# Performance work log

Hardware: AMD Instinct MI355X
Metric: run time of the kernel (lower is better)

## Reference

```python
import jax, jax.numpy as jnp
import numpy as np

NUM_HEADS = 16
THETA = 10000.0


def apply_rope(x, pos, theta):
    # x: [B, H, S, d], pos: [S] int
    d = x.shape[-1]
    inv_freq = theta ** (-jnp.arange(0, d, 2, dtype=jnp.float32) / d)  # [d/2]
    ang = pos.astype(jnp.float32)[:, None] * inv_freq  # [S, d/2]
    cos, sin = jnp.cos(ang), jnp.sin(ang)
    x1, x2 = x[..., 0::2], x[..., 1::2]
    out_even = x1 * cos - x2 * sin
    out_odd = x1 * sin + x2 * cos
    return jnp.stack([out_even, out_odd], axis=-1).reshape(x.shape)


def setup_inputs() -> dict:
    key = jax.random.key(0)
    ks = jax.random.split(key, 5)
    B, S, D = 4, 2048, 2048
    s = 1.0 / np.sqrt(D)
    return {
        "x": jax.random.normal(ks[0], (B, S, D), dtype=jnp.float32),
        "token_positions": jnp.arange(S, dtype=jnp.int32),
        "wq": jax.random.normal(ks[1], (D, D), dtype=jnp.float32) * s,
        "wk": jax.random.normal(ks[2], (D, D), dtype=jnp.float32) * s,
        "wv": jax.random.normal(ks[3], (D, D), dtype=jnp.float32) * s,
        "wo": jax.random.normal(ks[4], (D, D), dtype=jnp.float32) * s,
    }


def reference(x, token_positions, wq, wk, wv, wo):
    B, S, _ = x.shape
    H = NUM_HEADS
    dh = wq.shape[0] // H

    def proj(w):
        y = jnp.einsum('bsd,ed->bse', x, w)  # Linear: x @ W^T
        return y.reshape(B, S, H, dh).transpose(0, 2, 1, 3)  # [B,H,S,dh]

    Q, K, V = proj(wq), proj(wk), proj(wv)
    Q = apply_rope(Q, token_positions, THETA)
    K = apply_rope(K, token_positions, THETA)

    scores = jnp.einsum('bhqd,bhkd->bhqk', Q, K) / jnp.sqrt(jnp.float32(dh))
    causal = jnp.tril(jnp.ones((S, S), dtype=bool))
    scores = jnp.where(causal, scores, jnp.finfo(scores.dtype).min)
    attn = jax.nn.softmax(scores, axis=-1)
    out = jnp.einsum('bhqk,bhkd->bhqd', attn, V)
    out = out.transpose(0, 2, 1, 3).reshape(B, S, H * dh)
    return jnp.einsum('bsd,ed->bse', out, wo)
```

## Files before the change

### kernel.cpp

```cpp
#include <hip/hip_runtime.h>
#include <math.h>

typedef __bf16 bf16;
typedef bf16 bf16x8 __attribute__((ext_vector_type(8)));
typedef bf16 bf16x4v __attribute__((ext_vector_type(4)));
typedef float f32x4 __attribute__((ext_vector_type(4)));

#define BB 4
#define SS 2048
#define DD 2048
#define HH 16
#define DH 128

__device__ __forceinline__ void gload_lds16(const bf16* g, bf16* l) {
  __builtin_amdgcn_global_load_lds(
      (const __attribute__((address_space(1))) void*)g,
      (__attribute__((address_space(3))) void*)l, 16, 0, 0);
}

__global__ __launch_bounds__(256) void cast_kernel(const float* __restrict__ in,
                                                   bf16* __restrict__ out, int n4) {
  int i = blockIdx.x * blockDim.x + threadIdx.x;
  if (i < n4) {
    const float4 v = ((const float4*)in)[i];
    bf16x4v o = {(bf16)v.x, (bf16)v.y, (bf16)v.z, (bf16)v.w};
    ((bf16x4v*)out)[i] = o;
  }
}

__global__ __launch_bounds__(256) void cast4_kernel(const float* __restrict__ w0,
                                                    const float* __restrict__ w1,
                                                    const float* __restrict__ w2,
                                                    const float* __restrict__ w3,
                                                    bf16* __restrict__ out) {
  const int i = blockIdx.x * blockDim.x + threadIdx.x;
  const int per = (DD * DD) / 4;
  const int sel = i / per, off = i - sel * per;
  const float* src = (sel == 0) ? w0 : (sel == 1) ? w1 : (sel == 2) ? w2 : w3;
  const float4 v = ((const float4*)src)[off];
  bf16x4v o = {(bf16)v.x, (bf16)v.y, (bf16)v.z, (bf16)v.w};
  ((bf16x4v*)(out + (size_t)sel * DD * DD))[off] = o;
}

template <int MODE>
__global__ __launch_bounds__(256) void gemm_bt(const bf16* __restrict__ A,
                                               const bf16* __restrict__ Bw,
                                               bf16* __restrict__ Cb,
                                               float* __restrict__ Cf,
                                               const int* __restrict__ pos,
                                               int M, int N, int K) {
  __shared__ alignas(16) bf16 lA[128 * 64];
  __shared__ alignas(16) bf16 lB[128 * 64];
  const int tid = threadIdx.x;
  const int wave = tid >> 6, lane = tid & 63;
  const int quad = lane >> 4, l15 = lane & 15;
  const int m0 = blockIdx.y * 128, n0 = blockIdx.x * 128;
  const int wm = (wave >> 1) * 64, wn = (wave & 1) * 64;

  f32x4 acc[4][4] = {};

  for (int k0 = 0; k0 < K; k0 += 64) {
    __syncthreads();
#pragma unroll
    for (int i = 0; i < 4; ++i) {
      const int p = (wave * 4 + i) * 64 + lane;
      const int r = p >> 3, c = p & 7;
      gload_lds16(A + (size_t)(m0 + r) * K + k0 + c * 8, lA + (size_t)(wave * 4 + i) * 512);
      gload_lds16(Bw + (size_t)(n0 + r) * K + k0 + c * 8, lB + (size_t)(wave * 4 + i) * 512);
    }
    __syncthreads();
#pragma unroll
    for (int kk = 0; kk < 2; ++kk) {
      bf16x8 af[4], bfr[4];
#pragma unroll
      for (int t = 0; t < 4; ++t)
        af[t] = *(const bf16x8*)(lA + (wm + t * 16 + l15) * 64 + kk * 32 + quad * 8);
#pragma unroll
      for (int t = 0; t < 4; ++t)
        bfr[t] = *(const bf16x8*)(lB + (wn + t * 16 + l15) * 64 + kk * 32 + quad * 8);
#pragma unroll
      for (int mt = 0; mt < 4; ++mt)
#pragma unroll
        for (int nt = 0; nt < 4; ++nt)
          acc[mt][nt] = __builtin_amdgcn_mfma_f32_16x16x32_bf16(af[mt], bfr[nt], acc[mt][nt], 0, 0, 0);
    }
  }

  float ps[4][4];
  if (MODE == 0) {
#pragma unroll
    for (int mt = 0; mt < 4; ++mt)
#pragma unroll
      for (int r = 0; r < 4; ++r)
        ps[mt][r] = (float)pos[(m0 + wm + mt * 16 + quad * 4 + r) & (SS - 1)];
  }

#pragma unroll
  for (int nt = 0; nt < 4; ++nt) {
    const int col = n0 + wn + nt * 16 + l15;
    float invf = 0.f, sgn = 0.f;
    if (MODE == 0) {
      const int d = col & (DH - 1);
      invf = exp2f((float)(d >> 1) * (-13.28771238f / 64.0f));
      sgn = (d & 1) ? 1.0f : -1.0f;
    }
#pragma unroll
    for (int mt = 0; mt < 4; ++mt) {
#pragma unroll
      for (int r = 0; r < 4; ++r) {
        const int row = m0 + wm + mt * 16 + quad * 4 + r;
        float v = acc[mt][nt][r];
        if (MODE == 0) {
          const float partner = __shfl_xor(v, 1);
          float sn, cn;
          __sincosf(ps[mt][r] * invf, &sn, &cn);
          v = fmaf(partner, sgn * sn, v * cn);
          const int b = row >> 11, s = row & (SS - 1);
          const int h = col >> 7, d = col & (DH - 1);
          Cb[((((size_t)b * HH + h) * SS + s) << 7) + d] = (bf16)v;
        } else if (MODE == 1) {
          const int b = row >> 11, s = row & (SS - 1);
          const int h = col >> 7, d = col & (DH - 1);
          Cb[(((size_t)b * HH + h) * DH + d) * SS + s] = (bf16)v;
        } else {
          Cf[(size_t)row * N + col] = v;
        }
      }
    }
  }
}

__global__ __launch_bounds__(256, 2) void flash_attn(const bf16* __restrict__ Q,
                                                     const bf16* __restrict__ Kg,
                                                     const bf16* __restrict__ Vt,
                                                     bf16* __restrict__ O) {
  __shared__ alignas(16) bf16 lK[2][64 * 128];
  __shared__ alignas(16) bf16 lP[4][32 * 64];

  const int tid = threadIdx.x;
  const int wave = tid >> 6, lane = tid & 63;
  const int quad = lane >> 4, l15 = lane & 15;
  const int swz = l15 & 7;

  const int lin = blockIdx.y * gridDim.x + blockIdx.x;
  const int bh = ((lin & 7) << 3) | ((lin >> 3) & 7);
  const int q0 = (15 - (lin >> 6)) * 128;

  const bf16* Qh = Q + (size_t)bh * SS * DH;
  const bf16* Kh = Kg + (size_t)bh * SS * DH;
  const bf16* Vh = Vt + (size_t)bh * DH * SS;
  const int nkb = (q0 >> 6) + 2;
  const int qrow0 = q0 + wave * 32;

  bf16x8 qf[2][4];
#pragma unroll
  for (int qt = 0; qt < 2; ++qt)
#pragma unroll
    for (int t = 0; t < 4; ++t)
      qf[qt][t] = *(const bf16x8*)(Qh + (size_t)(qrow0 + qt * 16 + l15) * DH + t * 32 + quad * 8);

  bf16* lPw = &lP[wave][0];
  const float cs = 0.12751649736f;
  const float MSTAT = 20.0f;
  float lsum[2] = {0.f, 0.f};
  f32x4 oacc[2][8] = {};
  int cur = 0;

  auto stage = [&](int b, int kb) {
#pragma unroll
    for (int j = 0; j < 4; ++j) {
      const int c = tid + j * 256;
      const int kr = c >> 4;
      gload_lds16(Kh + (size_t)(kb * 64 + kr) * DH + (((c & 15) ^ (kr & 7)) * 8),
                  &lK[b][0] + (size_t)(wave * 64 + j * 256) * 8);
    }
  };

  auto kv_iter = [&](int kb, bool masked) {
    int ktlim = 3;
    if (masked) {
      ktlim = (qrow0 + 31 - kb * 64) >> 4;
      if (ktlim < 0) return;
      if (ktlim > 3) ktlim = 3;
    }
    const bf16* kcur = &lK[cur][0];

    f32x4 sacc[2][4];
#pragma unroll
    for (int qt = 0; qt < 2; ++qt)
#pragma unroll
      for (int kt = 0; kt < 4; ++kt) sacc[qt][kt] = (f32x4){0.f, 0.f, 0.f, 0.f};
    __builtin_amdgcn_s_setprio(1);
#pragma unroll
    for (int kt = 0; kt < 4; ++kt) {
      if (kt <= ktlim) {
#pragma unroll
        for (int t = 0; t < 4; ++t) {
          const bf16x8 kfrag =
              *(const bf16x8*)(kcur + (kt * 16 + l15) * 128 + (((t * 4 + quad) ^ swz) * 8));
          sacc[0][kt] = __builtin_amdgcn_mfma_f32_16x16x32_bf16(kfrag, qf[0][t], sacc[0][kt], 0, 0, 0);
          sacc[1][kt] = __builtin_amdgcn_mfma_f32_16x16x32_bf16(kfrag, qf[1][t], sacc[1][kt], 0, 0, 0);
        }
      }
    }
    __builtin_amdgcn_s_setprio(0);

#pragma unroll
    for (int kt = 0; kt < 4; ++kt) {
#pragma unroll
      for (int qt = 0; qt < 2; ++qt) {
        bf16x4v pk = {(bf16)0.f, (bf16)0.f, (bf16)0.f, (bf16)0.f};
        if (kt <= ktlim) {
          float ls = 0.f;
#pragma unroll
          for (int r = 0; r < 4; ++r) {
            float e = exp2f(fmaf(sacc[qt][kt][r], cs, -MSTAT));
            if (masked) {
              const int key = kb * 64 + kt * 16 + quad * 4 + r;
              if (key > qrow0 + qt * 16 + l15) e = 0.f;
            }
            ls += e;
            pk[r] = (bf16)e;
          }
          lsum[qt] += ls;
        }
        *(bf16x4v*)(lPw + (qt * 16 + l15) * 64 + (((kt * 2 + (quad >> 1)) ^ swz) * 8) +
                    (quad & 1) * 4) = pk;
      }
    }

    bf16x8 pa[2][2];
#pragma unroll
    for (int qt = 0; qt < 2; ++qt)
#pragma unroll
      for (int kc = 0; kc < 2; ++kc)
        pa[qt][kc] = *(const bf16x8*)(lPw + (qt * 16 + l15) * 64 + (((kc * 4 + quad) ^ swz) * 8));

    __builtin_amdgcn_s_setprio(1);
#pragma unroll
    for (int g = 0; g < 2; ++g) {
      bf16x8 vf[4][2];
#pragma unroll
      for (int d2 = 0; d2 < 4; ++d2)
#pragma unroll
        for (int kc = 0; kc < 2; ++kc)
          vf[d2][kc] = *(const bf16x8*)(Vh + (size_t)((g * 4 + d2) * 16 + l15) * SS + kb * 64 +
                                        kc * 32 + quad * 8);
#pragma unroll
      for (int d2 = 0; d2 < 4; ++d2)
#pragma unroll
        for (int kc = 0; kc < 2; ++kc) {
          oacc[0][g * 4 + d2] =
              __builtin_amdgcn_mfma_f32_16x16x32_bf16(pa[0][kc], vf[d2][kc], oacc[0][g * 4 + d2], 0, 0, 0);
          oacc[1][g * 4 + d2] =
              __builtin_amdgcn_mfma_f32_16x16x32_bf16(pa[1][kc], vf[d2][kc], oacc[1][g * 4 + d2], 0, 0, 0);
        }
    }
    __builtin_amdgcn_s_setprio(0);
  };

  stage(0, 0);
  __syncthreads();

  for (int kb = 0; kb < nkb - 1; ++kb) {
    stage(cur ^ 1, kb + 1);
    kv_iter(kb, kb + 2 >= nkb);
    __syncthreads();
    cur ^= 1;
  }
  kv_iter(nkb - 1, true);

#pragma unroll
  for (int qt = 0; qt < 2; ++qt) {
    lsum[qt] += __shfl_xor(lsum[qt], 16);
    lsum[qt] += __shfl_xor(lsum[qt], 32);
  }

  const int b = bh >> 4, h = bh & 15;
#pragma unroll
  for (int qt = 0; qt < 2; ++qt) {
#pragma unroll
    for (int r = 0; r < 4; ++r) {
      const int qq = quad * 4 + r;
      const float il = 1.0f / __shfl(lsum[qt], qq);
      bf16* orow = O + ((size_t)b * SS + qrow0 + qt * 16 + qq) * DD + h * DH;
#pragma unroll
      for (int db = 0; db < 8; ++db) orow[db * 16 + l15] = (bf16)(oacc[qt][db][r] * il);
    }
  }
}

extern "C" void kernel_launch(void* const* d_in, const int* in_sizes, int n_in,
                              void* d_out, int out_size, void* d_ws, size_t ws_size,
                              hipStream_t stream) {
  (void)in_sizes; (void)n_in; (void)out_size; (void)ws_size;
  const float* x = (const float*)d_in[0];
  const int* pos = (const int*)d_in[1];
  const float* wq = (const float*)d_in[2];
  const float* wk = (const float*)d_in[3];
  const float* wv = (const float*)d_in[4];
  const float* wo = (const float*)d_in[5];
  float* out = (float*)d_out;

  bf16* xb  = (bf16*)d_ws;
  bf16* wqb = xb + (size_t)BB * SS * DD;
  bf16* wkb = wqb + (size_t)DD * DD;
  bf16* wvb = wkb + (size_t)DD * DD;
  bf16* wob = wvb + (size_t)DD * DD;
  bf16* Qb  = wob + (size_t)DD * DD;
  bf16* Kbf = Qb + (size_t)BB * SS * DD;
  bf16* Vtb = Kbf + (size_t)BB * SS * DD;
  bf16* Ob  = Vtb + (size_t)BB * SS * DD;

  const int nx = BB * SS * DD;
  cast_kernel<<<nx / 4 / 256, 256, 0, stream>>>(x, xb, nx / 4);
  cast4_kernel<<<DD * DD / 256, 256, 0, stream>>>(wq, wk, wv, wo, wqb);

  dim3 gg(DD / 128, (BB * SS) / 128);
  gemm_bt<0><<<gg, 256, 0, stream>>>(xb, wqb, Qb, nullptr, pos, BB * SS, DD, DD);
  gemm_bt<0><<<gg, 256, 0, stream>>>(xb, wkb, Kbf, nullptr, pos, BB * SS, DD, DD);
  gemm_bt<1><<<gg, 256, 0, stream>>>(xb, wvb, Vtb, nullptr, nullptr, BB * SS, DD, DD);

  flash_attn<<<dim3(SS / 128, BB * HH), 256, 0, stream>>>(Qb, Kbf, Vtb, Ob);

  gemm_bt<2><<<gg, 256, 0, stream>>>(Ob, wob, nullptr, out, nullptr, BB * SS, DD, DD);
}
```

Baseline: 730.3 us.

## Replace 128x128 GEMM with pipelined 256x256 tile kernel using swizzled LDS

Rewrites the projection GEMM as a 512-thread kernel computing 256x256 output tiles with a 4-deep LDS ring buffer and prefetch two K-steps ahead. It adds an XOR swizzle on LDS columns to reduce bank conflicts, block-index remapping for L2 locality, and explicit barrier, waitcnt and setprio scheduling to overlap global loads with MFMA work. The larger tile raises arithmetic intensity per loaded byte but uses many more accumulator registers and yields only 256 blocks per GEMM, which may limit occupancy and load balance.

```diff
diff --git a/kernel.cpp b/kernel.cpp
--- a/kernel.cpp
+++ b/kernel.cpp
@@ -43,61 +43,111 @@
 }
 
 template <int MODE>
-__global__ __launch_bounds__(256) void gemm_bt(const bf16* __restrict__ A,
-                                               const bf16* __restrict__ Bw,
-                                               bf16* __restrict__ Cb,
-                                               float* __restrict__ Cf,
-                                               const int* __restrict__ pos,
-                                               int M, int N, int K) {
-  __shared__ alignas(16) bf16 lA[128 * 64];
-  __shared__ alignas(16) bf16 lB[128 * 64];
+__global__ __launch_bounds__(512, 2) void gemm256(const bf16* __restrict__ A,
+                                                  const bf16* __restrict__ Bw,
+                                                  bf16* __restrict__ Cb,
+                                                  float* __restrict__ Cf,
+                                                  const int* __restrict__ pos,
+                                                  int M, int N, int K) {
+  __shared__ alignas(16) bf16 lds[4][2][256 * 32];
+
   const int tid = threadIdx.x;
   const int wave = tid >> 6, lane = tid & 63;
   const int quad = lane >> 4, l15 = lane & 15;
-  const int m0 = blockIdx.y * 128, n0 = blockIdx.x * 128;
-  const int wm = (wave >> 1) * 64, wn = (wave & 1) * 64;
-
-  f32x4 acc[4][4] = {};
-
-  for (int k0 = 0; k0 < K; k0 += 64) {
-    __syncthreads();
-#pragma unroll
-    for (int i = 0; i < 4; ++i) {
-      const int p = (wave * 4 + i) * 64 + lane;
-      const int r = p >> 3, c = p & 7;
-      gload_lds16(A + (size_t)(m0 + r) * K + k0 + c * 8, lA + (size_t)(wave * 4 + i) * 512);
-      gload_lds16(Bw + (size_t)(n0 + r) * K + k0 + c * 8, lB + (size_t)(wave * 4 + i) * 512);
-    }
-    __syncthreads();
-#pragma unroll
-    for (int kk = 0; kk < 2; ++kk) {
-      bf16x8 af[4], bfr[4];
-#pragma unroll
-      for (int t = 0; t < 4; ++t)
-        af[t] = *(const bf16x8*)(lA + (wm + t * 16 + l15) * 64 + kk * 32 + quad * 8);
-#pragma unroll
-      for (int t = 0; t < 4; ++t)
-        bfr[t] = *(const bf16x8*)(lB + (wn + t * 16 + l15) * 64 + kk * 32 + quad * 8);
-#pragma unroll
-      for (int mt = 0; mt < 4; ++mt)
-#pragma unroll
-        for (int nt = 0; nt < 4; ++nt)
-          acc[mt][nt] = __builtin_amdgcn_mfma_f32_16x16x32_bf16(af[mt], bfr[nt], acc[mt][nt], 0, 0, 0);
-    }
-  }
-
-  float ps[4][4];
+  const int wm = wave >> 2, wn = wave & 3;
+
+  const int lin = blockIdx.y * gridDim.x + blockIdx.x;
+  const int swz = (lin & 7) * 32 + (lin >> 3);
+  const int m0 = (swz >> 3) * 256, n0 = (swz & 7) * 256;
+
+  auto stage = [&](int buf, int ab, const bf16* src, int rbase, int u) {
+    bf16* dst = &lds[buf][ab][0];
+#pragma unroll
+    for (int j = 0; j < 2; ++j) {
+      const int c = wave * 128 + j * 64 + lane;
+      const int row = c >> 2;
+      const int k8 = (c & 3) ^ ((row >> 1) & 3);
+      gload_lds16(src + (size_t)(rbase + row) * K + u * 32 + k8 * 8,
+                  dst + (size_t)(wave * 128 + j * 64) * 8);
+    }
+  };
+
+  auto rdA = [&](int buf, int mf) -> bf16x8 {
+    const int row = wm * 128 + mf * 16 + l15;
+    return *(const bf16x8*)(&lds[buf][0][0] + row * 32 + ((quad ^ ((row >> 1) & 3)) * 8));
+  };
+  auto rdB = [&](int buf, int nf) -> bf16x8 {
+    const int row = wn * 64 + nf * 16 + l15;
+    return *(const bf16x8*)(&lds[buf][1][0] + row * 32 + ((quad ^ ((row >> 1) & 3)) * 8));
+  };
+
+  f32x4 acc[8][4] = {};
+  const int NT = K >> 5;
+
+  stage(0, 0, A, m0, 0);
+  stage(0, 1, Bw, n0, 0);
+  stage(1, 0, A, m0, 1);
+  stage(1, 1, Bw, n0, 1);
+  asm volatile("s_waitcnt vmcnt(4)" ::: "memory");
+  __builtin_amdgcn_s_barrier();
+  __builtin_amdgcn_sched_barrier(0);
+
+  bf16x8 af[4], bfr[4];
+  for (int t = 0; t < NT; ++t) {
+    const int buf = t & 3;
+    const bool pre = (t + 2 < NT);
+#pragma unroll
+    for (int mf = 0; mf < 4; ++mf) af[mf] = rdA(buf, mf);
+#pragma unroll
+    for (int nf = 0; nf < 4; ++nf) bfr[nf] = rdB(buf, nf);
+    if (pre) stage((t + 2) & 3, 0, A, m0, t + 2);
+    __builtin_amdgcn_sched_barrier(0);
+    __builtin_amdgcn_s_barrier();
+    asm volatile("s_waitcnt lgkmcnt(0)" ::: "memory");
+    __builtin_amdgcn_sched_barrier(0);
+    __builtin_amdgcn_s_setprio(1);
+#pragma unroll
+    for (int mf = 0; mf < 4; ++mf)
+#pragma unroll
+      for (int nf = 0; nf < 4; ++nf)
+        acc[mf][nf] = __builtin_amdgcn_mfma_f32_16x16x32_bf16(af[mf], bfr[nf], acc[mf][nf], 0, 0, 0);
+    __builtin_amdgcn_s_setprio(0);
+    __builtin_amdgcn_sched_barrier(0);
+    __builtin_amdgcn_s_barrier();
+    __builtin_amdgcn_sched_barrier(0);
+#pragma unroll
+    for (int mf = 0; mf < 4; ++mf) af[mf] = rdA(buf, mf + 4);
+    if (pre) stage((t + 2) & 3, 1, Bw, n0, t + 2);
+    __builtin_amdgcn_sched_barrier(0);
+    __builtin_amdgcn_s_barrier();
+    asm volatile("s_waitcnt lgkmcnt(0)" ::: "memory");
+    __builtin_amdgcn_sched_barrier(0);
+    __builtin_amdgcn_s_setprio(1);
+#pragma unroll
+    for (int mf = 0; mf < 4; ++mf)
+#pragma unroll
+      for (int nf = 0; nf < 4; ++nf)
+        acc[mf + 4][nf] = __builtin_amdgcn_mfma_f32_16x16x32_bf16(af[mf], bfr[nf], acc[mf + 4][nf], 0, 0, 0);
+    __builtin_amdgcn_s_setprio(0);
+    if (pre) asm volatile("s_waitcnt vmcnt(4)" ::: "memory");
+    else     asm volatile("s_waitcnt vmcnt(0)" ::: "memory");
+    __builtin_amdgcn_sched_barrier(0);
+    __builtin_amdgcn_s_barrier();
+    __builtin_amdgcn_sched_barrier(0);
+  }
+
+  float ps[8][4];
   if (MODE == 0) {
 #pragma unroll
-    for (int mt = 0; mt < 4; ++mt)
+    for (int mf = 0; mf < 8; ++mf)
 #pragma unroll
       for (int r = 0; r < 4; ++r)
-        ps[mt][r] = (float)pos[(m0 + wm + mt * 16 + quad * 4 + r) & (SS - 1)];
-  }
-
-#pragma unroll
-  for (int nt = 0; nt < 4; ++nt) {
-    const int col = n0 + wn + nt * 16 + l15;
+        ps[mf][r] = (float)pos[(m0 + wm * 128 + mf * 16 + quad * 4 + r) & (SS - 1)];
+  }
+
+#pragma unroll
+  for (int nf = 0; nf < 4; ++nf) {
+    const int col = n0 + wn * 64 + nf * 16 + l15;
     float invf = 0.f, sgn = 0.f;
     if (MODE == 0) {
       const int d = col & (DH - 1);
@@ -105,15 +155,15 @@
       sgn = (d & 1) ? 1.0f : -1.0f;
     }
 #pragma unroll
-    for (int mt = 0; mt < 4; ++mt) {
+    for (int mf = 0; mf < 8; ++mf) {
 #pragma unroll
       for (int r = 0; r < 4; ++r) {
-        const int row = m0 + wm + mt * 16 + quad * 4 + r;
-        float v = acc[mt][nt][r];
+        const int row = m0 + wm * 128 + mf * 16 + quad * 4 + r;
+        float v = acc[mf][nf][r];
         if (MODE == 0) {
           const float partner = __shfl_xor(v, 1);
           float sn, cn;
-          __sincosf(ps[mt][r] * invf, &sn, &cn);
+          __sincosf(ps[mf][r] * invf, &sn, &cn);
           v = fmaf(partner, sgn * sn, v * cn);
           const int b = row >> 11, s = row & (SS - 1);
           const int h = col >> 7, d = col & (DH - 1);
@@ -316,12 +366,12 @@
   cast_kernel<<<nx / 4 / 256, 256, 0, stream>>>(x, xb, nx / 4);
   cast4_kernel<<<DD * DD / 256, 256, 0, stream>>>(wq, wk, wv, wo, wqb);
 
-  dim3 gg(DD / 128, (BB * SS) / 128);
-  gemm_bt<0><<<gg, 256, 0, stream>>>(xb, wqb, Qb, nullptr, pos, BB * SS, DD, DD);
-  gemm_bt<0><<<gg, 256, 0, stream>>>(xb, wkb, Kbf, nullptr, pos, BB * SS, DD, DD);
-  gemm_bt<1><<<gg, 256, 0, stream>>>(xb, wvb, Vtb, nullptr, nullptr, BB * SS, DD, DD);
+  dim3 gg(DD / 256, (BB * SS) / 256);
+  gemm256<0><<<gg, 512, 0, stream>>>(xb, wqb, Qb, nullptr, pos, BB * SS, DD, DD);
+  gemm256<0><<<gg, 512, 0, stream>>>(xb, wkb, Kbf, nullptr, pos, BB * SS, DD, DD);
+  gemm256<1><<<gg, 512, 0, stream>>>(xb, wvb, Vtb, nullptr, nullptr, BB * SS, DD, DD);
 
   flash_attn<<<dim3(SS / 128, BB * HH), 256, 0, stream>>>(Qb, Kbf, Vtb, Ob);
 
-  gemm_bt<2><<<gg, 256, 0, stream>>>(Ob, wob, nullptr, out, nullptr, BB * SS, DD, DD);
-}
+  gemm256<2><<<gg, 512, 0, stream>>>(Ob, wob, nullptr, out, nullptr, BB * SS, DD, DD);
+}
```

After: 636.6 us. 1.15x faster.
